# Kernel tuning notes

Hardware: AMD Instinct MI355X
Metric: run time of the kernel (lower is better)

## Reference

```python
import jax, jax.numpy as jnp
import numpy as np

B, T, C, H = 8, 1024, 1024, 16
D = C // H  # head size 64
EPS = 1e-5

def layernorm(x, g, b):
    m = jnp.mean(x, axis=-1, keepdims=True)
    v = jnp.var(x, axis=-1, keepdims=True)
    return (x - m) * jax.lax.rsqrt(v + EPS) * g + b

def setup_inputs() -> dict:
    key = jax.random.key(0)
    ks = jax.random.split(key, 12)
    s = 1.0 / np.sqrt(C)
    return {
        "x": jax.random.normal(ks[0], (B, T, C), dtype=jnp.float32),
        "mask": jnp.ones((B, 1, 1, T), dtype=jnp.int32),
        "Wq": jax.random.normal(ks[1], (C, C), dtype=jnp.float32) * s,
        "Wk": jax.random.normal(ks[2], (C, C), dtype=jnp.float32) * s,
        "Wv": jax.random.normal(ks[3], (C, C), dtype=jnp.float32) * s,
        "Wo": jax.random.normal(ks[4], (C, C), dtype=jnp.float32) * s,
        "bo": jnp.zeros((C,), dtype=jnp.float32),
        "ln1_g": jnp.ones((C,), dtype=jnp.float32),
        "ln1_b": jnp.zeros((C,), dtype=jnp.float32),
        "ln3_g": jnp.ones((C,), dtype=jnp.float32),
        "ln3_b": jnp.zeros((C,), dtype=jnp.float32),
        "W1": jax.random.normal(ks[5], (C, 4 * C), dtype=jnp.float32) * s,
        "b1": jnp.zeros((4 * C,), dtype=jnp.float32),
        "W2": jax.random.normal(ks[6], (4 * C, C), dtype=jnp.float32) * (1.0 / np.sqrt(4 * C)),
        "b2": jnp.zeros((C,), dtype=jnp.float32),
    }

def reference(x, mask, Wq, Wk, Wv, Wo, bo, ln1_g, ln1_b, ln3_g, ln3_b, W1, b1, W2, b2):
    # --- self-attention sublayer (pre-LN, residual) ---
    xn = layernorm(x, ln1_g, ln1_b)                      # [B,T,C]
    q = (xn @ Wq).reshape(B, T, H, D)                    # [B,T,H,D]
    k = (xn @ Wk).reshape(B, T, H, D)
    v = (xn @ Wv).reshape(B, T, H, D)
    scores = jnp.einsum('bqhd,bkhd->bhqk', q, k) / np.sqrt(D)  # [B,H,T,T]
    scores = jnp.where(mask == 0, -jnp.inf, scores)      # padding mask [B,1,1,T] broadcasts
    attn = jax.nn.softmax(scores, axis=-1)               # dropout=0.0 -> identity
    o = jnp.einsum('bhqk,bkhd->bqhd', attn, v).reshape(B, T, C)
    x = x + o @ Wo + bo
    # --- feed-forward sublayer (pre-LN, residual) ---
    h = layernorm(x, ln3_g, ln3_b)
    ff = jax.nn.relu(h @ W1 + b1) @ W2 + b2
    return x + ff
```

## Files before the change

### kernel.cpp

```cpp
#include <hip/hip_runtime.h>
#include <stdint.h>

typedef unsigned short u16;
typedef __bf16 bf16x8 __attribute__((ext_vector_type(8)));
typedef float f32x4 __attribute__((ext_vector_type(4)));

#define B_ 8
#define T_ 1024
#define C_ 1024
#define H_ 16
#define D_ 64
#define M_TOT 8192
#define FF_ 4096

__device__ __forceinline__ u16 f2bf(float f) {
  union { float f; unsigned u; } c; c.f = f;
  unsigned u = c.u;
  return (u16)((u + 0x7FFFu + ((u >> 16) & 1u)) >> 16);
}

__device__ __forceinline__ void g2l16(const void* g, void* l) {
  __builtin_amdgcn_global_load_lds((const __attribute__((address_space(1))) void*)g,
                                   (__attribute__((address_space(3))) void*)l, 16, 0, 0);
}

__global__ __launch_bounds__(256) void trans_f32_bf16(const float* __restrict__ in,
                                                      u16* __restrict__ out, int R, int C) {
  __shared__ float t[32][33];
  int c0 = blockIdx.x * 32, r0 = blockIdx.y * 32;
  int tx = threadIdx.x & 31, ty = threadIdx.x >> 5;
#pragma unroll
  for (int i = ty; i < 32; i += 8)
    t[i][tx] = in[(size_t)(r0 + i) * C + c0 + tx];
  __syncthreads();
#pragma unroll
  for (int i = ty; i < 32; i += 8)
    out[(size_t)(c0 + i) * R + r0 + tx] = f2bf(t[tx][i]);
}

__global__ __launch_bounds__(256) void vtrans_bf16(const u16* __restrict__ v,
                                                   u16* __restrict__ vt) {
  __shared__ u16 t[64][66];
  int bh = blockIdx.y;
  int b = bh >> 4, h = bh & 15;
  int t0 = blockIdx.x * 64;
  int tx = threadIdx.x & 63, w = threadIdx.x >> 6;
#pragma unroll
  for (int i = w; i < 64; i += 4)
    t[i][tx] = v[(size_t)(b * T_ + t0 + i) * C_ + h * D_ + tx];
  __syncthreads();
#pragma unroll
  for (int d = w; d < 64; d += 4)
    vt[((size_t)bh * D_ + d) * T_ + t0 + tx] = t[tx][d];
}

__global__ __launch_bounds__(256) void ln_f32_bf16(const float* __restrict__ x,
                                                   const float* __restrict__ g,
                                                   const float* __restrict__ bt,
                                                   u16* __restrict__ out) {
  int row = blockIdx.x, tid = threadIdx.x;
  const float4* xr = (const float4*)(x + (size_t)row * C_);
  float4 a = xr[tid];
  float s = a.x + a.y + a.z + a.w;
  float ss = a.x * a.x + a.y * a.y + a.z * a.z + a.w * a.w;
#pragma unroll
  for (int m = 1; m < 64; m <<= 1) { s += __shfl_xor(s, m); ss += __shfl_xor(ss, m); }
  __shared__ float red[8];
  int wave = tid >> 6, lane = tid & 63;
  if (lane == 0) { red[wave] = s; red[wave + 4] = ss; }
  __syncthreads();
  s = red[0] + red[1] + red[2] + red[3];
  ss = red[4] + red[5] + red[6] + red[7];
  float mean = s * (1.0f / C_);
  float rstd = rsqrtf(ss * (1.0f / C_) - mean * mean + 1e-5f);
  float4 gg = ((const float4*)g)[tid];
  float4 bb = ((const float4*)bt)[tid];
  u16* op = out + (size_t)row * C_ + tid * 4;
  op[0] = f2bf((a.x - mean) * rstd * gg.x + bb.x);
  op[1] = f2bf((a.y - mean) * rstd * gg.y + bb.y);
  op[2] = f2bf((a.z - mean) * rstd * gg.z + bb.z);
  op[3] = f2bf((a.w - mean) * rstd * gg.w + bb.w);
}

template <int EPI>
__global__ __launch_bounds__(256) void gemm_bf16(const u16* __restrict__ A,
                                                 const u16* __restrict__ BT,
                                                 u16* __restrict__ outb, float* __restrict__ outf,
                                                 const float* __restrict__ bias,
                                                 const float* __restrict__ resid,
                                                 int M, int N, int K) {
  __shared__ u16 As[128 * 32];
  __shared__ u16 Bs[128 * 32];
  int tid = threadIdx.x, wave = tid >> 6, lane = tid & 63;
  int m0 = blockIdx.y * 128, n0 = blockIdx.x * 128;
  int wr = wave >> 1, wc = wave & 1;
  int frow = lane & 15, fk = (lane >> 4) * 8;
  f32x4 acc[4][4] = {};
  for (int k0 = 0; k0 < K; k0 += 32) {
    __syncthreads();
#pragma unroll
    for (int i = 0; i < 2; i++) {
      int c = i * 256 + tid;
      const u16* ga = A + (size_t)(m0 + (c >> 2)) * K + k0 + (c & 3) * 8;
      const u16* gb = BT + (size_t)(n0 + (c >> 2)) * K + k0 + (c & 3) * 8;
      g2l16(ga, As + (i * 256 + wave * 64) * 8);
      g2l16(gb, Bs + (i * 256 + wave * 64) * 8);
    }
    asm volatile("s_waitcnt vmcnt(0)" ::: "memory");
    __syncthreads();
    bf16x8 af[4], bfr[4];
#pragma unroll
    for (int m = 0; m < 4; m++) af[m] = *(const bf16x8*)(As + (wr * 64 + m * 16 + frow) * 32 + fk);
#pragma unroll
    for (int n = 0; n < 4; n++) bfr[n] = *(const bf16x8*)(Bs + (wc * 64 + n * 16 + frow) * 32 + fk);
#pragma unroll
    for (int m = 0; m < 4; m++)
#pragma unroll
      for (int n = 0; n < 4; n++)
        acc[m][n] = __builtin_amdgcn_mfma_f32_16x16x32_bf16(af[m], bfr[n], acc[m][n], 0, 0, 0);
  }
#pragma unroll
  for (int m = 0; m < 4; m++)
#pragma unroll
    for (int n = 0; n < 4; n++)
#pragma unroll
      for (int r = 0; r < 4; r++) {
        int row = m0 + wr * 64 + m * 16 + (lane >> 4) * 4 + r;
        int col = n0 + wc * 64 + n * 16 + (lane & 15);
        float v = acc[m][n][r];
        if (EPI == 0) {
          outb[(size_t)row * N + col] = f2bf(v);
        } else if (EPI == 1) {
          v += bias[col];
          v = fmaxf(v, 0.f);
          outb[(size_t)row * N + col] = f2bf(v);
        } else {
          v += bias[col] + resid[(size_t)row * N + col];
          outf[(size_t)row * N + col] = v;
        }
      }
}

__global__ __launch_bounds__(256) void attn_kernel(const u16* __restrict__ q,
                                                   const u16* __restrict__ k,
                                                   const u16* __restrict__ vt,
                                                   const int* __restrict__ mask,
                                                   u16* __restrict__ o) {
  __shared__ __attribute__((aligned(16))) u16 kbuf[2][64 * 64];
  __shared__ __attribute__((aligned(16))) u16 vbuf[2][64 * 64];
  __shared__ __attribute__((aligned(16))) u16 plds[4][16 * 72];

  int tid = threadIdx.x, wave = tid >> 6, lane = tid & 63;
  int qt = blockIdx.x;
  int bh = blockIdx.y;
  int b = bh >> 4, h = bh & 15;
  const size_t base = ((size_t)b * T_) * C_ + h * D_;
  int l15 = lane & 15, g = lane >> 4;

  int qrow = qt * 64 + wave * 16 + l15;
  int dk = g * 8;
  bf16x8 qf0 = *(const bf16x8*)(q + base + (size_t)qrow * C_ + dk);
  bf16x8 qf1 = *(const bf16x8*)(q + base + (size_t)qrow * C_ + dk + 32);

  const u16* vtb = vt + (size_t)bh * D_ * T_;

  int c0 = tid, r0s = c0 >> 3, cc0 = c0 & 7, sc0 = cc0 ^ (r0s & 7);
  int c1 = 256 + tid, r1s = c1 >> 3, cc1 = c1 & 7, sc1 = cc1 ^ (r1s & 7);
  const u16* ksrc0 = k + base + (size_t)r0s * C_ + sc0 * 8;
  const u16* ksrc1 = k + base + (size_t)r1s * C_ + sc1 * 8;
  const u16* vsrc0 = vtb + (size_t)r0s * T_ + sc0 * 8;
  const u16* vsrc1 = vtb + (size_t)r1s * T_ + sc1 * 8;
  int dst0 = (0 * 256 + wave * 64) * 8;
  int dst1 = (1 * 256 + wave * 64) * 8;

  f32x4 oacc[4] = {};
  float mrun[4], lrun[4];
#pragma unroll
  for (int r = 0; r < 4; r++) { mrun[r] = -1e30f; lrun[r] = 0.f; }

  u16* pw = plds[wave];
  const int wsw = g * 8;
  const int rsw = ((l15 >> 2) & 3) * 8;
  const int swz0 = (g ^ (l15 & 7)) * 8;
  const int swz1 = ((g + 4) ^ (l15 & 7)) * 8;

  {
    g2l16(ksrc0, kbuf[0] + dst0);
    g2l16(ksrc1, kbuf[0] + dst1);
    g2l16(vsrc0, vbuf[0] + dst0);
    g2l16(vsrc1, vbuf[0] + dst1);
  }
  asm volatile("s_waitcnt vmcnt(0)" ::: "memory");
  __syncthreads();

  for (int kt = 0; kt < T_ / 64; ++kt) {
    int cur = kt & 1;
    if (kt < T_ / 64 - 1) {
      int nxt = cur ^ 1;
      size_t ko = (size_t)(kt + 1) * 64 * C_;
      size_t vo = (size_t)(kt + 1) * 64;
      g2l16(ksrc0 + ko, kbuf[nxt] + dst0);
      g2l16(ksrc1 + ko, kbuf[nxt] + dst1);
      g2l16(vsrc0 + vo, vbuf[nxt] + dst0);
      g2l16(vsrc1 + vo, vbuf[nxt] + dst1);
    }
    int mv[4];
#pragma unroll
    for (int c = 0; c < 4; c++) mv[c] = mask[b * T_ + kt * 64 + c * 16 + l15];

    const u16* kb = kbuf[cur];
    f32x4 s[4];
#pragma unroll
    for (int c = 0; c < 4; c++) {
      const u16* kp = kb + (c * 16 + l15) * 64;
      bf16x8 k0 = *(const bf16x8*)(kp + swz0);
      bf16x8 k1 = *(const bf16x8*)(kp + swz1);
      f32x4 a = {};
      a = __builtin_amdgcn_mfma_f32_16x16x32_bf16(qf0, k0, a, 0, 0, 0);
      a = __builtin_amdgcn_mfma_f32_16x16x32_bf16(qf1, k1, a, 0, 0, 0);
#pragma unroll
      for (int r = 0; r < 4; r++) a[r] = mv[c] ? a[r] * 0.125f : -1e30f;
      s[c] = a;
    }
    float tmax[4];
#pragma unroll
    for (int r = 0; r < 4; r++)
      tmax[r] = fmaxf(fmaxf(s[0][r], s[1][r]), fmaxf(s[2][r], s[3][r]));
#pragma unroll
    for (int m = 1; m < 16; m <<= 1)
#pragma unroll
      for (int r = 0; r < 4; r++) tmax[r] = fmaxf(tmax[r], __shfl_xor(tmax[r], m));
    float alpha[4];
#pragma unroll
    for (int r = 0; r < 4; r++) {
      float nm = fmaxf(mrun[r], tmax[r]);
      alpha[r] = __expf(mrun[r] - nm);
      mrun[r] = nm;
    }
    float psum[4] = {0.f, 0.f, 0.f, 0.f};
#pragma unroll
    for (int c = 0; c < 4; c++)
#pragma unroll
      for (int r = 0; r < 4; r++) {
        float p = __expf(s[c][r] - mrun[r]);
        s[c][r] = p;
        psum[r] += p;
      }
#pragma unroll
    for (int m = 1; m < 16; m <<= 1)
#pragma unroll
      for (int r = 0; r < 4; r++) psum[r] += __shfl_xor(psum[r], m);
#pragma unroll
    for (int r = 0; r < 4; r++) lrun[r] = lrun[r] * alpha[r] + psum[r];
#pragma unroll
    for (int n = 0; n < 4; n++)
#pragma unroll
      for (int r = 0; r < 4; r++) oacc[n][r] *= alpha[r];
#pragma unroll
    for (int c = 0; c < 4; c++)
#pragma unroll
      for (int r = 0; r < 4; r++)
        pw[(4 * g + r) * 72 + ((c * 16 + l15) ^ wsw)] = f2bf(s[c][r]);
    bf16x8 pa0 = *(const bf16x8*)(pw + l15 * 72 + (0 * 32 + (g * 8 ^ rsw)));
    bf16x8 pa1 = *(const bf16x8*)(pw + l15 * 72 + (1 * 32 + (g * 8 ^ rsw)));
    const u16* vb2 = vbuf[cur];
#pragma unroll
    for (int n = 0; n < 4; n++) {
      const u16* vp = vb2 + (n * 16 + l15) * 64;
      bf16x8 v0 = *(const bf16x8*)(vp + swz0);
      bf16x8 v1 = *(const bf16x8*)(vp + swz1);
      oacc[n] = __builtin_amdgcn_mfma_f32_16x16x32_bf16(pa0, v0, oacc[n], 0, 0, 0);
      oacc[n] = __builtin_amdgcn_mfma_f32_16x16x32_bf16(pa1, v1, oacc[n], 0, 0, 0);
    }
    asm volatile("s_waitcnt vmcnt(0)" ::: "memory");
    __syncthreads();
  }
#pragma unroll
  for (int n = 0; n < 4; n++)
#pragma unroll
    for (int r = 0; r < 4; r++) {
      int row = qt * 64 + wave * 16 + g * 4 + r;
      o[((size_t)b * T_ + row) * C_ + h * D_ + n * 16 + l15] =
          f2bf(oacc[n][r] / lrun[r]);
    }
}

extern "C" void kernel_launch(void* const* d_in, const int* in_sizes, int n_in,
                              void* d_out, int out_size, void* d_ws, size_t ws_size,
                              hipStream_t stream) {
  const float* x    = (const float*)d_in[0];
  const int*   mask = (const int*)d_in[1];
  const float* Wq   = (const float*)d_in[2];
  const float* Wk   = (const float*)d_in[3];
  const float* Wv   = (const float*)d_in[4];
  const float* Wo   = (const float*)d_in[5];
  const float* bo   = (const float*)d_in[6];
  const float* ln1g = (const float*)d_in[7];
  const float* ln1b = (const float*)d_in[8];
  const float* ln3g = (const float*)d_in[9];
  const float* ln3b = (const float*)d_in[10];
  const float* W1   = (const float*)d_in[11];
  const float* b1   = (const float*)d_in[12];
  const float* W2   = (const float*)d_in[13];
  const float* b2   = (const float*)d_in[14];
  float* out = (float*)d_out;

  char* ws = (char*)d_ws;
  const size_t MB = 1024 * 1024;
  u16* WqT = (u16*)(ws + 0 * MB);
  u16* WkT = (u16*)(ws + 2 * MB);
  u16* WvT = (u16*)(ws + 4 * MB);
  u16* WoT = (u16*)(ws + 6 * MB);
  u16* W1T = (u16*)(ws + 8 * MB);
  u16* W2T = (u16*)(ws + 16 * MB);
  u16* xn  = (u16*)(ws + 24 * MB);
  u16* qb  = (u16*)(ws + 40 * MB);
  u16* kb  = (u16*)(ws + 56 * MB);
  u16* vb  = (u16*)(ws + 72 * MB);
  u16* ob  = (u16*)(ws + 88 * MB);
  float* x2 = (float*)(ws + 104 * MB);
  u16* vT  = xn;
  u16* hb  = xn;
  u16* ff1 = qb;

  dim3 blk(256);
  trans_f32_bf16<<<dim3(32, 32), blk, 0, stream>>>(Wq, WqT, 1024, 1024);
  trans_f32_bf16<<<dim3(32, 32), blk, 0, stream>>>(Wk, WkT, 1024, 1024);
  trans_f32_bf16<<<dim3(32, 32), blk, 0, stream>>>(Wv, WvT, 1024, 1024);
  trans_f32_bf16<<<dim3(32, 32), blk, 0, stream>>>(Wo, WoT, 1024, 1024);
  trans_f32_bf16<<<dim3(128, 32), blk, 0, stream>>>(W1, W1T, 1024, 4096);
  trans_f32_bf16<<<dim3(32, 128), blk, 0, stream>>>(W2, W2T, 4096, 1024);
  ln_f32_bf16<<<8192, blk, 0, stream>>>(x, ln1g, ln1b, xn);
  gemm_bf16<0><<<dim3(8, 64), blk, 0, stream>>>(xn, WqT, qb, nullptr, nullptr, nullptr, 8192, 1024, 1024);
  gemm_bf16<0><<<dim3(8, 64), blk, 0, stream>>>(xn, WkT, kb, nullptr, nullptr, nullptr, 8192, 1024, 1024);
  gemm_bf16<0><<<dim3(8, 64), blk, 0, stream>>>(xn, WvT, vb, nullptr, nullptr, nullptr, 8192, 1024, 1024);
  vtrans_bf16<<<dim3(16, 128), blk, 0, stream>>>(vb, vT);
  attn_kernel<<<dim3(16, 128), blk, 0, stream>>>(qb, kb, vT, mask, ob);
  gemm_bf16<2><<<dim3(8, 64), blk, 0, stream>>>(ob, WoT, nullptr, x2, bo, x, 8192, 1024, 1024);
  ln_f32_bf16<<<8192, blk, 0, stream>>>(x2, ln3g, ln3b, hb);
  gemm_bf16<1><<<dim3(32, 64), blk, 0, stream>>>(hb, W1T, ff1, nullptr, b1, nullptr, 8192, 4096, 1024);
  gemm_bf16<2><<<dim3(8, 64), blk, 0, stream>>>(ff1, W2T, nullptr, out, b2, x2, 8192, 1024, 4096);
}
```

Before: 632.8 us.

## Fuse QKV projections and switch to double-buffered 256x256 GEMM tiles

Concatenates the transposed Wq/Wk/Wv into one weight and runs a single fused QKV GEMM into a strided qkv buffer, which attention and the V-transpose now read. Replaces the 128x128 single-buffered GEMM with a 512-thread 256x256 tile kernel that double-buffers global-to-LDS loads with partial vmcnt waits, uses XOR-swizzled LDS and raises priority around MFMAs. The goal is more data reuse per tile and load/compute overlap. In exchange it uses more LDS and registers, and larger tiles mean fewer blocks, e.g. only 128 blocks for the N=1024 GEMMs, which may underfill the GPU.

```diff
diff --git a/kernel.cpp b/kernel.cpp
--- a/kernel.cpp
+++ b/kernel.cpp
@@ -10,8 +10,7 @@
 #define C_ 1024
 #define H_ 16
 #define D_ 64
-#define M_TOT 8192
-#define FF_ 4096
+#define QKS 3072
 
 __device__ __forceinline__ u16 f2bf(float f) {
   union { float f; unsigned u; } c; c.f = f;
@@ -38,7 +37,7 @@
     out[(size_t)(c0 + i) * R + r0 + tx] = f2bf(t[tx][i]);
 }
 
-__global__ __launch_bounds__(256) void vtrans_bf16(const u16* __restrict__ v,
+__global__ __launch_bounds__(256) void vtrans_bf16(const u16* __restrict__ qkv,
                                                    u16* __restrict__ vt) {
   __shared__ u16 t[64][66];
   int bh = blockIdx.y;
@@ -47,7 +46,7 @@
   int tx = threadIdx.x & 63, w = threadIdx.x >> 6;
 #pragma unroll
   for (int i = w; i < 64; i += 4)
-    t[i][tx] = v[(size_t)(b * T_ + t0 + i) * C_ + h * D_ + tx];
+    t[i][tx] = qkv[(size_t)(b * T_ + t0 + i) * QKS + 2048 + h * D_ + tx];
   __syncthreads();
 #pragma unroll
   for (int d = w; d < 64; d += 4)
@@ -83,51 +82,78 @@
 }
 
 template <int EPI>
-__global__ __launch_bounds__(256) void gemm_bf16(const u16* __restrict__ A,
-                                                 const u16* __restrict__ BT,
-                                                 u16* __restrict__ outb, float* __restrict__ outf,
-                                                 const float* __restrict__ bias,
-                                                 const float* __restrict__ resid,
-                                                 int M, int N, int K) {
-  __shared__ u16 As[128 * 32];
-  __shared__ u16 Bs[128 * 32];
-  int tid = threadIdx.x, wave = tid >> 6, lane = tid & 63;
-  int m0 = blockIdx.y * 128, n0 = blockIdx.x * 128;
-  int wr = wave >> 1, wc = wave & 1;
-  int frow = lane & 15, fk = (lane >> 4) * 8;
-  f32x4 acc[4][4] = {};
-  for (int k0 = 0; k0 < K; k0 += 32) {
-    __syncthreads();
-#pragma unroll
-    for (int i = 0; i < 2; i++) {
-      int c = i * 256 + tid;
-      const u16* ga = A + (size_t)(m0 + (c >> 2)) * K + k0 + (c & 3) * 8;
-      const u16* gb = BT + (size_t)(n0 + (c >> 2)) * K + k0 + (c & 3) * 8;
-      g2l16(ga, As + (i * 256 + wave * 64) * 8);
-      g2l16(gb, Bs + (i * 256 + wave * 64) * 8);
-    }
-    asm volatile("s_waitcnt vmcnt(0)" ::: "memory");
-    __syncthreads();
-    bf16x8 af[4], bfr[4];
-#pragma unroll
-    for (int m = 0; m < 4; m++) af[m] = *(const bf16x8*)(As + (wr * 64 + m * 16 + frow) * 32 + fk);
-#pragma unroll
-    for (int n = 0; n < 4; n++) bfr[n] = *(const bf16x8*)(Bs + (wc * 64 + n * 16 + frow) * 32 + fk);
-#pragma unroll
-    for (int m = 0; m < 4; m++)
-#pragma unroll
-      for (int n = 0; n < 4; n++)
-        acc[m][n] = __builtin_amdgcn_mfma_f32_16x16x32_bf16(af[m], bfr[n], acc[m][n], 0, 0, 0);
+__global__ __launch_bounds__(512, 2) void gemm256(const u16* __restrict__ A,
+                                                  const u16* __restrict__ BT,
+                                                  u16* __restrict__ outb, float* __restrict__ outf,
+                                                  const float* __restrict__ bias,
+                                                  const float* __restrict__ resid,
+                                                  int M, int N, int K) {
+  __shared__ __attribute__((aligned(16))) u16 Abuf[2][256 * 32];
+  __shared__ __attribute__((aligned(16))) u16 Bbuf[2][256 * 32];
+  const int tid = threadIdx.x, wave = tid >> 6, lane = tid & 63;
+  const int l15 = lane & 15, g = lane >> 4;
+  const int wr = wave >> 2, wc = wave & 3;
+  const int m0 = blockIdx.y * 256, n0 = blockIdx.x * 256;
+  const int srow = tid >> 2;
+  const int sc = (tid & 3) ^ (srow & 3);
+  const u16* a0 = A + (size_t)(m0 + srow) * K + sc * 8;
+  const u16* b0 = BT + (size_t)(n0 + srow) * K + sc * 8;
+  const int dst = wave * 512;
+  const int rsw = l15 & 3;
+  const int NT = K >> 5;
+
+#pragma unroll
+  for (int j = 0; j < 2; j++) {
+    g2l16(a0 + (size_t)j * 128 * K, Abuf[0] + j * 4096 + dst);
+    g2l16(b0 + (size_t)j * 128 * K, Bbuf[0] + j * 4096 + dst);
   }
-#pragma unroll
-  for (int m = 0; m < 4; m++)
-#pragma unroll
-    for (int n = 0; n < 4; n++)
+  f32x4 acc[8][4] = {};
+  for (int kt = 0; kt < NT; ++kt) {
+    const int cur = kt & 1;
+    if (kt + 1 < NT) {
+      const size_t ko = (size_t)(kt + 1) * 32;
+#pragma unroll
+      for (int j = 0; j < 2; j++) {
+        g2l16(a0 + (size_t)j * 128 * K + ko, Abuf[cur ^ 1] + j * 4096 + dst);
+        g2l16(b0 + (size_t)j * 128 * K + ko, Bbuf[cur ^ 1] + j * 4096 + dst);
+      }
+      asm volatile("s_waitcnt vmcnt(4)" ::: "memory");
+    } else {
+      asm volatile("s_waitcnt vmcnt(0)" ::: "memory");
+    }
+    __builtin_amdgcn_s_barrier();
+    const u16* ab = Abuf[cur];
+    const u16* bb = Bbuf[cur];
+    bf16x8 bfr[4];
+#pragma unroll
+    for (int nn = 0; nn < 4; nn++)
+      bfr[nn] = *(const bf16x8*)(bb + (wc * 64 + nn * 16 + l15) * 32 + ((g ^ rsw) * 8));
+#pragma unroll
+    for (int q = 0; q < 4; q++) {
+      bf16x8 af[2];
+#pragma unroll
+      for (int i = 0; i < 2; i++)
+        af[i] = *(const bf16x8*)(ab + (wr * 128 + (2 * q + i) * 16 + l15) * 32 + ((g ^ rsw) * 8));
+      __builtin_amdgcn_s_setprio(1);
+#pragma unroll
+      for (int i = 0; i < 2; i++)
+#pragma unroll
+        for (int nn = 0; nn < 4; nn++)
+          acc[2 * q + i][nn] =
+              __builtin_amdgcn_mfma_f32_16x16x32_bf16(af[i], bfr[nn], acc[2 * q + i][nn], 0, 0, 0);
+      __builtin_amdgcn_s_setprio(0);
+    }
+    __builtin_amdgcn_s_barrier();
+  }
+#pragma unroll
+  for (int mm = 0; mm < 8; mm++)
+#pragma unroll
+    for (int nn = 0; nn < 4; nn++)
 #pragma unroll
       for (int r = 0; r < 4; r++) {
-        int row = m0 + wr * 64 + m * 16 + (lane >> 4) * 4 + r;
-        int col = n0 + wc * 64 + n * 16 + (lane & 15);
-        float v = acc[m][n][r];
+        int row = m0 + wr * 128 + mm * 16 + g * 4 + r;
+        int col = n0 + wc * 64 + nn * 16 + l15;
+        float v = acc[mm][nn][r];
         if (EPI == 0) {
           outb[(size_t)row * N + col] = f2bf(v);
         } else if (EPI == 1) {
@@ -141,8 +167,7 @@
       }
 }
 
-__global__ __launch_bounds__(256) void attn_kernel(const u16* __restrict__ q,
-                                                   const u16* __restrict__ k,
+__global__ __launch_bounds__(256) void attn_kernel(const u16* __restrict__ qkv,
                                                    const u16* __restrict__ vt,
                                                    const int* __restrict__ mask,
                                                    u16* __restrict__ o) {
@@ -154,20 +179,21 @@
   int qt = blockIdx.x;
   int bh = blockIdx.y;
   int b = bh >> 4, h = bh & 15;
-  const size_t base = ((size_t)b * T_) * C_ + h * D_;
   int l15 = lane & 15, g = lane >> 4;
 
   int qrow = qt * 64 + wave * 16 + l15;
   int dk = g * 8;
-  bf16x8 qf0 = *(const bf16x8*)(q + base + (size_t)qrow * C_ + dk);
-  bf16x8 qf1 = *(const bf16x8*)(q + base + (size_t)qrow * C_ + dk + 32);
+  const u16* qp = qkv + (size_t)(b * T_ + qrow) * QKS + h * D_;
+  bf16x8 qf0 = *(const bf16x8*)(qp + dk);
+  bf16x8 qf1 = *(const bf16x8*)(qp + dk + 32);
 
   const u16* vtb = vt + (size_t)bh * D_ * T_;
+  const size_t kbase = (size_t)(b * T_) * QKS + 1024 + h * D_;
 
   int c0 = tid, r0s = c0 >> 3, cc0 = c0 & 7, sc0 = cc0 ^ (r0s & 7);
   int c1 = 256 + tid, r1s = c1 >> 3, cc1 = c1 & 7, sc1 = cc1 ^ (r1s & 7);
-  const u16* ksrc0 = k + base + (size_t)r0s * C_ + sc0 * 8;
-  const u16* ksrc1 = k + base + (size_t)r1s * C_ + sc1 * 8;
+  const u16* ksrc0 = qkv + kbase + (size_t)r0s * QKS + sc0 * 8;
+  const u16* ksrc1 = qkv + kbase + (size_t)r1s * QKS + sc1 * 8;
   const u16* vsrc0 = vtb + (size_t)r0s * T_ + sc0 * 8;
   const u16* vsrc1 = vtb + (size_t)r1s * T_ + sc1 * 8;
   int dst0 = (0 * 256 + wave * 64) * 8;
@@ -197,7 +223,7 @@
     int cur = kt & 1;
     if (kt < T_ / 64 - 1) {
       int nxt = cur ^ 1;
-      size_t ko = (size_t)(kt + 1) * 64 * C_;
+      size_t ko = (size_t)(kt + 1) * 64 * QKS;
       size_t vo = (size_t)(kt + 1) * 64;
       g2l16(ksrc0 + ko, kbuf[nxt] + dst0);
       g2l16(ksrc1 + ko, kbuf[nxt] + dst1);
@@ -307,37 +333,34 @@
 
   char* ws = (char*)d_ws;
   const size_t MB = 1024 * 1024;
-  u16* WqT = (u16*)(ws + 0 * MB);
-  u16* WkT = (u16*)(ws + 2 * MB);
-  u16* WvT = (u16*)(ws + 4 * MB);
-  u16* WoT = (u16*)(ws + 6 * MB);
-  u16* W1T = (u16*)(ws + 8 * MB);
-  u16* W2T = (u16*)(ws + 16 * MB);
-  u16* xn  = (u16*)(ws + 24 * MB);
-  u16* qb  = (u16*)(ws + 40 * MB);
-  u16* kb  = (u16*)(ws + 56 * MB);
-  u16* vb  = (u16*)(ws + 72 * MB);
-  u16* ob  = (u16*)(ws + 88 * MB);
-  float* x2 = (float*)(ws + 104 * MB);
+  u16* WqkvT = (u16*)(ws + 0 * MB);
+  u16* WoT   = (u16*)(ws + 6 * MB);
+  u16* W1T   = (u16*)(ws + 8 * MB);
+  u16* W2T   = (u16*)(ws + 16 * MB);
+  u16* xn    = (u16*)(ws + 24 * MB);
+  u16* qkv   = (u16*)(ws + 40 * MB);
+  u16* ob    = (u16*)(ws + 88 * MB);
+  float* x2  = (float*)(ws + 104 * MB);
   u16* vT  = xn;
   u16* hb  = xn;
-  u16* ff1 = qb;
-
-  dim3 blk(256);
-  trans_f32_bf16<<<dim3(32, 32), blk, 0, stream>>>(Wq, WqT, 1024, 1024);
-  trans_f32_bf16<<<dim3(32, 32), blk, 0, stream>>>(Wk, WkT, 1024, 1024);
-  trans_f32_bf16<<<dim3(32, 32), blk, 0, stream>>>(Wv, WvT, 1024, 1024);
-  trans_f32_bf16<<<dim3(32, 32), blk, 0, stream>>>(Wo, WoT, 1024, 1024);
-  trans_f32_bf16<<<dim3(128, 32), blk, 0, stream>>>(W1, W1T, 1024, 4096);
-  trans_f32_bf16<<<dim3(32, 128), blk, 0, stream>>>(W2, W2T, 4096, 1024);
-  ln_f32_bf16<<<8192, blk, 0, stream>>>(x, ln1g, ln1b, xn);
-  gemm_bf16<0><<<dim3(8, 64), blk, 0, stream>>>(xn, WqT, qb, nullptr, nullptr, nullptr, 8192, 1024, 1024);
-  gemm_bf16<0><<<dim3(8, 64), blk, 0, stream>>>(xn, WkT, kb, nullptr, nullptr, nullptr, 8192, 1024, 1024);
-  gemm_bf16<0><<<dim3(8, 64), blk, 0, stream>>>(xn, WvT, vb, nullptr, nullptr, nullptr, 8192, 1024, 1024);
-  vtrans_bf16<<<dim3(16, 128), blk, 0, stream>>>(vb, vT);
-  attn_kernel<<<dim3(16, 128), blk, 0, stream>>>(qb, kb, vT, mask, ob);
-  gemm_bf16<2><<<dim3(8, 64), blk, 0, stream>>>(ob, WoT, nullptr, x2, bo, x, 8192, 1024, 1024);
-  ln_f32_bf16<<<8192, blk, 0, stream>>>(x2, ln3g, ln3b, hb);
-  gemm_bf16<1><<<dim3(32, 64), blk, 0, stream>>>(hb, W1T, ff1, nullptr, b1, nullptr, 8192, 4096, 1024);
-  gemm_bf16<2><<<dim3(8, 64), blk, 0, stream>>>(ff1, W2T, nullptr, out, b2, x2, 8192, 1024, 4096);
-}
+  u16* ff1 = qkv;
+
+  dim3 b256(256), b512(512);
+  trans_f32_bf16<<<dim3(32, 32), b256, 0, stream>>>(Wq, WqkvT, 1024, 1024);
+  trans_f32_bf16<<<dim3(32, 32), b256, 0, stream>>>(Wk, WqkvT + 1024 * 1024, 1024, 1024);
+  trans_f32_bf16<<<dim3(32, 32), b256, 0, stream>>>(Wv, WqkvT + 2048 * 1024, 1024, 1024);
+  trans_f32_bf16<<<dim3(32, 32), b256, 0, stream>>>(Wo, WoT, 1024, 1024);
+  trans_f32_bf16<<<dim3(128, 32), b256, 0, stream>>>(W1, W1T, 1024, 4096);
+  trans_f32_bf16<<<dim3(32, 128), b256, 0, stream>>>(W2, W2T, 4096, 1024);
+  ln_f32_bf16<<<8192, b256, 0, stream>>>(x, ln1g, ln1b, xn);
+  gemm256<0><<<dim3(12, 32), b512, 0, stream>>>(xn, WqkvT, qkv, nullptr, nullptr, nullptr,
+                                                8192, 3072, 1024);
+  vtrans_bf16<<<dim3(16, 128), b256, 0, stream>>>(qkv, vT);
+  attn_kernel<<<dim3(16, 128), b256, 0, stream>>>(qkv, vT, mask, ob);
+  gemm256<2><<<dim3(4, 32), b512, 0, stream>>>(ob, WoT, nullptr, x2, bo, x, 8192, 1024, 1024);
+  ln_f32_bf16<<<8192, b256, 0, stream>>>(x2, ln3g, ln3b, hb);
+  gemm256<1><<<dim3(16, 32), b512, 0, stream>>>(hb, W1T, ff1, nullptr, b1, nullptr,
+                                                8192, 4096, 1024);
+  gemm256<2><<<dim3(4, 32), b512, 0, stream>>>(ff1, W2T, nullptr, out, b2, x2,
+                                               8192, 1024, 4096);
+}
```

Measured after the change: 705.4 us. 11.5% more time.
